# Kernel optimization log

Hardware: AMD Instinct MI355X
Metric: run time of the kernel (lower is better)

The kernel has to match this reference:

```python
import jax, jax.numpy as jnp
import numpy as np

BS, N, HID, INPUT, PREK, KHOP = 16, 1024, 64, 64, 4, 3
D = 2 * HID            # hidden channel dim (128)
F = 2 * INPUT          # input feature dim (128)
C = F + D              # graphconv input channels (256)
NM = KHOP + 1          # num_metrics = k_hop*n_supports + 1 with n_supports=1
PI = 3.141592653589793
EMB_RANGE = (12.0 + 2.0) / HID   # (gamma + epsilon) / hidden_size


def setup_inputs() -> dict:
    key = jax.random.key(0)
    ks = jax.random.split(key, 12)
    inputs = jax.random.normal(ks[0], (BS, N, F), jnp.float32)
    # per-sample dynamic support; scale by 1/N to keep Chebyshev recursion stable
    supports = jax.random.uniform(ks[1], (BS, N, N), jnp.float32) / N
    hidden_states = jax.random.normal(ks[2], (BS, PREK, N, D), jnp.float32)
    W = jax.random.normal(ks[3], (D, D), jnp.float32) * 0.02
    b = jax.random.normal(ks[4], (N, D), jnp.float32) * 0.02
    R = jax.random.normal(ks[5], (PREK, N, HID), jnp.float32) * 0.02
    gc_w = jax.random.normal(ks[6], (D, C * NM), jnp.float32) * 0.02
    gc_b = jax.random.normal(ks[7], (D,), jnp.float32) * 0.02
    ev_att_w = jax.random.normal(ks[8], (1, N * D), jnp.float32) * 0.001
    ev_att_b = jax.random.normal(ks[9], (1,), jnp.float32) * 0.02
    att_w = jax.random.normal(ks[10], (1, N * D), jnp.float32) * 0.001
    att_b = jax.random.normal(ks[11], (1,), jnp.float32) * 0.02
    return {"inputs": inputs, "supports": supports, "hidden_states": hidden_states,
            "W": W, "b": b, "R": R, "gc_w": gc_w, "gc_b": gc_b,
            "ev_att_w": ev_att_w, "ev_att_b": ev_att_b,
            "att_w": att_w, "att_b": att_b}


def reference(inputs, supports, hidden_states, W, b, R, gc_w, gc_b,
              ev_att_w, ev_att_b, att_w, att_b):
    bs, k, n, d = hidden_states.shape
    # split inputs / last hidden into real/imag halves
    re_in, im_in = jnp.split(inputs, 2, axis=-1)          # [bs,n,INPUT]
    preH = hidden_states[:, -1]                           # [bs,n,d]
    re_p, im_p = jnp.split(preH, 2, axis=-1)              # [bs,n,HID]
    conv_in = jnp.concatenate([re_in, re_p, im_in, im_p], axis=-1)  # [bs,n,C]

    # diffusion graph conv (Chebyshev-style recursion over single batched support)
    x0 = conv_in
    x1 = jnp.matmul(supports, x0)                         # [bs,n,C]
    xs = [x0, x1]
    for _ in range(2, KHOP + 1):
        x2 = 2.0 * jnp.matmul(supports, x1) - x0
        xs.append(x2)
        x0, x1 = x1, x2
    # stack K metrics, permute to [bs,n,C,K], flatten (channel-major, step-minor)
    x = jnp.stack(xs, axis=0).transpose(1, 2, 3, 0).reshape(bs, n, C * NM)
    gco = x @ gc_w.T + gc_b                               # [bs,n,d]

    # EvolutionCell attention over g=1 group (kept for faithfulness)
    xe = gco.reshape(bs, 1, n * d)
    se = xe @ ev_att_w.T + ev_att_b                       # [bs,1,1]
    we = jax.nn.softmax(se, axis=1)
    conv_out = (xe * we).sum(axis=1).reshape(bs, n, d)

    # leaky_relu_ (slope 0.01)
    conv_out = jnp.where(conv_out >= 0, conv_out, 0.01 * conv_out)

    # RotatE-style complex phase rotation of hidden states
    phase = R / (EMB_RANGE / PI)                          # [k,n,HID]
    re_rel, im_rel = jnp.cos(phase), jnp.sin(phase)
    re_h, im_h = jnp.split(hidden_states, 2, axis=-1)     # [bs,k,n,HID]
    re_new = re_rel * re_h - im_rel * im_h
    im_new = im_rel * re_h + re_rel * im_h
    new_states = jnp.concatenate([re_new, im_new], axis=-1)  # [bs,k,n,d]

    # attention over k memory slots
    xa = new_states.reshape(bs, k, n * d)
    sa = xa @ att_w.T + att_b                             # [bs,k,1]
    wa = jax.nn.softmax(sa, axis=1)
    att = (xa * wa).sum(axis=1).reshape(bs, n, d)

    output = conv_out @ W + b[None] + att                 # [bs,n,d]
    new_hidden = jnp.concatenate([hidden_states[:, 1:], output[:, None]], axis=1)
    return output, new_hidden
```

## Files before the change

### kernel.cpp

```cpp
#include <hip/hip_runtime.h>
#include <cstddef>

constexpr float PHASE_SCALE = (float)(3.141592653589793 / ((12.0 + 2.0) / 64.0));

typedef __bf16 bf16;
typedef __bf16 bf16x4 __attribute__((ext_vector_type(4)));
typedef __bf16 bf16x8 __attribute__((ext_vector_type(8)));
typedef float floatx4 __attribute__((ext_vector_type(4)));

#define GLOAD_LDS16(gp, lp) __builtin_amdgcn_global_load_lds( \
    (const __attribute__((address_space(1))) void*)(gp),      \
    (__attribute__((address_space(3))) void*)(lp), 16, 0, 0)

#define VM_WAIT(n) asm volatile("s_waitcnt vmcnt(" #n ")" ::: "memory")

__global__ __launch_bounds__(256) void prep_kernel(
    const float4* __restrict__ S, bf16* __restrict__ Sbf,
    const float* __restrict__ R,
    const float* __restrict__ gcw, const float* __restrict__ W,
    bf16* __restrict__ gtAll, bf16* __restrict__ WT,
    const float* __restrict__ inp, const float* __restrict__ hs,
    bf16* __restrict__ xRow, bf16* __restrict__ xT0,
    const float* __restrict__ attw, float* __restrict__ part)
{
    __shared__ bf16 tile[64][65];
    __shared__ float red[256];
    const int bid = blockIdx.x;
    const int tid = threadIdx.x;

    if (bid < 576) {
        int gi = bid * 256 + tid;
        if (gi < 131072) {
            int m = gi >> 15;
            int rem = gi & 32767;
            int d = rem >> 8;
            int c = rem & 255;
            gtAll[gi] = (bf16)gcw[(size_t)d * 1024 + c * 4 + m];
        } else {
            int r = gi - 131072;
            int n = r >> 7, k = r & 127;
            WT[r] = (bf16)W[(size_t)k * 128 + n];
        }
    } else if (bid < 1088) {
        int bid3 = bid - 576;
        int bk = bid3 & 63;
        int k = bk & 3;
        int chunk = bid3 >> 6;
        const float* hbase = hs + (size_t)bk * 131072;
        float acc = 0.f;
        for (int idx = tid; idx < 2048; idx += 256) {
            int h4 = (idx & 15) * 4;
            int n = chunk * 128 + (idx >> 4);
            float4 rr  = *(const float4*)(R + (size_t)k * 65536 + n * 64 + h4);
            float4 re  = *(const float4*)(hbase + (size_t)n * 128 + h4);
            float4 im  = *(const float4*)(hbase + (size_t)n * 128 + 64 + h4);
            float4 wre = *(const float4*)(attw + (size_t)n * 128 + h4);
            float4 wim = *(const float4*)(attw + (size_t)n * 128 + 64 + h4);
            float sv, cv;
            __sincosf(rr.x * PHASE_SCALE, &sv, &cv);
            acc += (cv * re.x - sv * im.x) * wre.x + (sv * re.x + cv * im.x) * wim.x;
            __sincosf(rr.y * PHASE_SCALE, &sv, &cv);
            acc += (cv * re.y - sv * im.y) * wre.y + (sv * re.y + cv * im.y) * wim.y;
            __sincosf(rr.z * PHASE_SCALE, &sv, &cv);
            acc += (cv * re.z - sv * im.z) * wre.z + (sv * re.z + cv * im.z) * wim.z;
            __sincosf(rr.w * PHASE_SCALE, &sv, &cv);
            acc += (cv * re.w - sv * im.w) * wre.w + (sv * re.w + cv * im.w) * wim.w;
        }
        red[tid] = acc;
        __syncthreads();
        for (int s2 = 128; s2 > 0; s2 >>= 1) {
            if (tid < s2) red[tid] += red[tid + s2];
            __syncthreads();
        }
        if (tid == 0) part[bk * 8 + chunk] = red[0];
    } else if (bid < 2112) {
        int lin = bid - 1088;
        int b = lin >> 6, by = (lin >> 2) & 15, bx = lin & 3;
        int n0 = by * 64, c0 = bx * 64;
        const float* base = (bx & 1) ? (hs + (((size_t)b * 4 + 3) * 1024) * 128)
                                     : (inp + ((size_t)b * 1024) * 128);
        int soff = (bx >> 1) * 64;
        #pragma unroll
        for (int it = 0; it < 2; ++it) {
            int unit = it * 256 + tid;
            int nl = unit >> 3, cs = unit & 7;
            const float* src = base + (size_t)(n0 + nl) * 128 + soff + cs * 8;
            float4 a0 = *(const float4*)src;
            float4 a1 = *(const float4*)(src + 4);
            bf16x8 o;
            o[0] = (bf16)a0.x; o[1] = (bf16)a0.y; o[2] = (bf16)a0.z; o[3] = (bf16)a0.w;
            o[4] = (bf16)a1.x; o[5] = (bf16)a1.y; o[6] = (bf16)a1.z; o[7] = (bf16)a1.w;
            *(bf16x8*)(xRow + ((size_t)b * 1024 + n0 + nl) * 256 + c0 + cs * 8) = o;
            #pragma unroll
            for (int e = 0; e < 8; ++e) tile[nl][cs * 8 + e] = o[e];
        }
        __syncthreads();
        #pragma unroll
        for (int it = 0; it < 4; ++it) {
            int unit = it * 256 + tid;
            int ng = unit & 15, cc = unit >> 4;
            bf16x4 v;
            #pragma unroll
            for (int r = 0; r < 4; ++r) v[r] = tile[ng * 4 + r][cc];
            *(bf16x4*)(xT0 + ((size_t)b * 256 + c0 + cc) * 1024 + n0 + ng * 4) = v;
        }
    } else {
        int gi = (bid - 2112) * 256 + tid;
        const float4* Sp = S + (size_t)gi * 2;
        float4 v0 = Sp[0];
        float4 v1 = Sp[1];
        bf16x8 o;
        o[0] = (bf16)v0.x; o[1] = (bf16)v0.y; o[2] = (bf16)v0.z; o[3] = (bf16)v0.w;
        o[4] = (bf16)v1.x; o[5] = (bf16)v1.y; o[6] = (bf16)v1.z; o[7] = (bf16)v1.w;
        *(bf16x8*)(Sbf + (size_t)gi * 8) = o;
    }
}

__global__ __launch_bounds__(512) void cheb_mfma_kernel(
    const bf16* __restrict__ S, const bf16* __restrict__ xT,
    const bf16* __restrict__ xTprev, bf16* __restrict__ outT,
    const bf16* __restrict__ xRow0, const bf16* __restrict__ gtA,
    const bf16* __restrict__ gt0, float* __restrict__ gcoF,
    float alpha, int accumulate)
{
    __shared__ char smem[122880];
    const int f = blockIdx.x;
    const int b = (f & 7) + 8 * ((f >> 3) & 1);
    const int n0 = (f >> 4) * 64;
    const int tid = threadIdx.x;
    const int wave = tid >> 6, lane = tid & 63;
    const int wr = (wave & 3) * 16;
    const int wc = (wave >> 2) * 128;
    const int l15 = lane & 15, quad = lane >> 4;
    const int lrow = lane >> 3;
    const int segsw = (lane & 7) ^ lrow;

    const bf16* Sb = S + (size_t)b * 1048576;
    const bf16* xb = xT + (size_t)b * 262144;

    auto stage = [&](int buf, int k0) {
        bf16* dA = (bf16*)(smem + buf * 40960);
        bf16* dB = dA + 4096;
        {
            const bf16* gp = Sb + (size_t)(n0 + wave * 8 + lrow) * 1024 + k0 + segsw * 8;
            GLOAD_LDS16(gp, dA + wave * 8 * 64);
        }
        #pragma unroll
        for (int v = 0; v < 4; ++v) {
            int cq = wave * 32 + v * 8;
            const bf16* gp = xb + (size_t)(cq + lrow) * 1024 + k0 + segsw * 8;
            GLOAD_LDS16(gp, dB + cq * 64);
        }
    };

    floatx4 acc[8] = {};
    stage(0, 0);
    stage(1, 64);
    for (int i = 0; i < 16; ++i) {
        if (i < 15) { VM_WAIT(5); } else { VM_WAIT(0); }
        __builtin_amdgcn_s_barrier();
        __builtin_amdgcn_sched_barrier(0);
        const bf16* lA = (const bf16*)(smem + (i % 3) * 40960);
        const bf16* lB = lA + 4096;
        #pragma unroll
        for (int ks = 0; ks < 2; ++ks) {
            int row = wr + l15;
            int aslot = (ks * 4 + quad) ^ (row & 7);
            bf16x8 af = *(const bf16x8*)(lA + row * 64 + aslot * 8);
            #pragma unroll
            for (int j = 0; j < 8; ++j) {
                int col = wc + j * 16 + l15;
                int bslot = (ks * 4 + quad) ^ (col & 7);
                bf16x8 bfr = *(const bf16x8*)(lB + col * 64 + bslot * 8);
                acc[j] = __builtin_amdgcn_mfma_f32_16x16x32_bf16(af, bfr, acc[j], 0, 0, 0);
            }
        }
        if (i + 2 < 16) stage((i + 2) % 3, (i + 2) * 64);
    }

    const bf16* pT = xTprev ? xTprev + (size_t)b * 262144 : nullptr;
    bf16* oT = outT ? outT + (size_t)b * 262144 : nullptr;
    bf16x4 xo[8];
    #pragma unroll
    for (int j = 0; j < 8; ++j) {
        int col = wc + j * 16 + l15;
        float v[4];
        #pragma unroll
        for (int r = 0; r < 4; ++r) v[r] = alpha * acc[j][r];
        if (pT) {
            bf16x4 pp = *(const bf16x4*)(pT + (size_t)col * 1024 + n0 + wr + quad * 4);
            #pragma unroll
            for (int r = 0; r < 4; ++r) v[r] -= (float)pp[r];
        }
        #pragma unroll
        for (int r = 0; r < 4; ++r) xo[j][r] = (bf16)v[r];
        if (oT) *(bf16x4*)(oT + (size_t)col * 1024 + n0 + wr + quad * 4) = xo[j];
    }

    __syncthreads();
    bf16* ldsX = (bf16*)smem;
    #pragma unroll
    for (int j = 0; j < 8; ++j) {
        int col = wc + j * 16 + l15;
        #pragma unroll
        for (int r = 0; r < 4; ++r)
            ldsX[(wr + quad * 4 + r) * 264 + col] = xo[j][r];
    }
    __syncthreads();

    const int dbase = (wave >> 2) * 64;
    floatx4 a2[4] = {};
    for (int k2 = 0; k2 < 256; k2 += 32) {
        bf16x8 af = *(const bf16x8*)(ldsX + (wr + l15) * 264 + k2 + quad * 8);
        #pragma unroll
        for (int j = 0; j < 4; ++j) {
            int dcol = dbase + j * 16 + l15;
            bf16x8 bfr = *(const bf16x8*)(gtA + (size_t)dcol * 256 + k2 + quad * 8);
            a2[j] = __builtin_amdgcn_mfma_f32_16x16x32_bf16(af, bfr, a2[j], 0, 0, 0);
        }
    }
    if (xRow0) {
        for (int k2 = 0; k2 < 256; k2 += 32) {
            bf16x8 af = *(const bf16x8*)(xRow0 + ((size_t)b * 1024 + n0 + wr + l15) * 256 + k2 + quad * 8);
            #pragma unroll
            for (int j = 0; j < 4; ++j) {
                int dcol = dbase + j * 16 + l15;
                bf16x8 bfr = *(const bf16x8*)(gt0 + (size_t)dcol * 256 + k2 + quad * 8);
                a2[j] = __builtin_amdgcn_mfma_f32_16x16x32_bf16(af, bfr, a2[j], 0, 0, 0);
            }
        }
    }
    #pragma unroll
    for (int j = 0; j < 4; ++j) {
        int dcol = dbase + j * 16 + l15;
        #pragma unroll
        for (int r = 0; r < 4; ++r) {
            size_t idx = ((size_t)b * 1024 + n0 + wr + quad * 4 + r) * 128 + dcol;
            if (accumulate) gcoF[idx] += a2[j][r];
            else            gcoF[idx]  = a2[j][r];
        }
    }
}

__global__ __launch_bounds__(256) void final_kernel(
    const float* __restrict__ gcoF, const float* __restrict__ gcb,
    const bf16* __restrict__ WT, const float* __restrict__ bvec,
    const float* __restrict__ hs, const float* __restrict__ R,
    const float* __restrict__ part, const float* __restrict__ attb,
    float* __restrict__ out, float* __restrict__ newh)
{
    const int m0 = blockIdx.x * 64;
    const int b = m0 >> 10, n0 = m0 & 1023;
    const int tid = threadIdx.x;
    const int wave = tid >> 6, lane = tid & 63;
    const int l15 = lane & 15, quad = lane >> 4;

    const int arow = m0 + wave * 16 + l15;
    floatx4 acc[8] = {};
    #pragma unroll
    for (int k0 = 0; k0 < 128; k0 += 32) {
        int kk = k0 + quad * 8;
        float4 p0 = *(const float4*)(gcoF + (size_t)arow * 128 + kk);
        float4 p1 = *(const float4*)(gcoF + (size_t)arow * 128 + kk + 4);
        float4 g0 = *(const float4*)(gcb + kk);
        float4 g1 = *(const float4*)(gcb + kk + 4);
        float vv[8] = {p0.x + g0.x, p0.y + g0.y, p0.z + g0.z, p0.w + g0.w,
                       p1.x + g1.x, p1.y + g1.y, p1.z + g1.z, p1.w + g1.w};
        bf16x8 af;
        #pragma unroll
        for (int e = 0; e < 8; ++e) {
            float v = vv[e];
            af[e] = (bf16)(v >= 0.f ? v : 0.01f * v);
        }
        #pragma unroll
        for (int j = 0; j < 8; ++j) {
            bf16x8 bfr = *(const bf16x8*)(WT + (size_t)(j * 16 + l15) * 128 + kk);
            acc[j] = __builtin_amdgcn_mfma_f32_16x16x32_bf16(af, bfr, acc[j], 0, 0, 0);
        }
    }

    float sa[4], mx = -1e30f;
    #pragma unroll
    for (int k = 0; k < 4; ++k) {
        float s = attb[0];
        #pragma unroll
        for (int c = 0; c < 8; ++c) s += part[(b * 4 + k) * 8 + c];
        sa[k] = s;
        mx = fmaxf(mx, s);
    }
    float den = 0.f;
    #pragma unroll
    for (int k = 0; k < 4; ++k) { sa[k] = __expf(sa[k] - mx); den += sa[k]; }
    float inv = 1.f / den;
    #pragma unroll
    for (int k = 0; k < 4; ++k) sa[k] *= inv;

    #pragma unroll
    for (int jj = 0; jj < 4; ++jj) {
        int hcol = jj * 16 + l15;
        #pragma unroll
        for (int r = 0; r < 4; ++r) {
            int n = n0 + wave * 16 + quad * 4 + r;
            float attRe = 0.f, attIm = 0.f;
            #pragma unroll
            for (int k = 0; k < 4; ++k) {
                const float* hb = hs + (((size_t)(b * 4 + k) * 1024 + n) * 128);
                float re = hb[hcol], im = hb[64 + hcol];
                float s, c;
                __sincosf(R[(size_t)k * 65536 + n * 64 + hcol] * PHASE_SCALE, &s, &c);
                attRe += sa[k] * (c * re - s * im);
                attIm += sa[k] * (s * re + c * im);
                if (k >= 1) {
                    size_t nb = (size_t)b * 524288 + (size_t)(k - 1) * 131072 + (size_t)n * 128;
                    newh[nb + hcol] = re;
                    newh[nb + 64 + hcol] = im;
                }
            }
            size_t ob = (size_t)(m0 + wave * 16 + quad * 4 + r) * 128;
            float oRe = acc[jj][r]     + bvec[(size_t)n * 128 + hcol]      + attRe;
            float oIm = acc[jj + 4][r] + bvec[(size_t)n * 128 + 64 + hcol] + attIm;
            out[ob + hcol] = oRe;
            out[ob + 64 + hcol] = oIm;
            size_t nb3 = (size_t)b * 524288 + 393216 + (size_t)n * 128;
            newh[nb3 + hcol] = oRe;
            newh[nb3 + 64 + hcol] = oIm;
        }
    }
}

extern "C" void kernel_launch(void* const* d_in, const int* in_sizes, int n_in,
                              void* d_out, int out_size, void* d_ws, size_t ws_size,
                              hipStream_t stream) {
    const float* inp  = (const float*)d_in[0];
    const float* sup  = (const float*)d_in[1];
    const float* hs   = (const float*)d_in[2];
    const float* W    = (const float*)d_in[3];
    const float* bvec = (const float*)d_in[4];
    const float* R    = (const float*)d_in[5];
    const float* gcw  = (const float*)d_in[6];
    const float* gcb  = (const float*)d_in[7];
    const float* attw = (const float*)d_in[10];
    const float* attb = (const float*)d_in[11];

    float* out  = (float*)d_out;
    float* newh = out + 2097152;
    bf16*  Sbf  = (bf16*)newh;

    char* w = (char*)d_ws;
    bf16*  xT0   = (bf16*)(w);
    bf16*  xT1   = (bf16*)(w + 8388608);
    bf16*  xT2   = (bf16*)(w + 16777216);
    bf16*  xRow  = (bf16*)(w + 25165824);
    float* gcoF  = (float*)(w + 33554432);
    bf16*  gtAll = (bf16*)(w + 41943040);
    bf16*  WT    = (bf16*)(w + 42205184);
    float* part  = (float*)(w + 42237952);

    prep_kernel<<<10304, 256, 0, stream>>>((const float4*)sup, Sbf, R, gcw, W,
                                           gtAll, WT, inp, hs, xRow, xT0, attw, part);

    cheb_mfma_kernel<<<256, 512, 0, stream>>>(Sbf, xT0, nullptr, xT1,
                                              xRow, gtAll + 32768, gtAll, gcoF, 1.0f, 0);
    cheb_mfma_kernel<<<256, 512, 0, stream>>>(Sbf, xT1, xT0, xT2,
                                              nullptr, gtAll + 2 * 32768, nullptr, gcoF, 2.0f, 1);
    cheb_mfma_kernel<<<256, 512, 0, stream>>>(Sbf, xT2, xT1, nullptr,
                                              nullptr, gtAll + 3 * 32768, nullptr, gcoF, 2.0f, 1);

    final_kernel<<<256, 256, 0, stream>>>(gcoF, gcb, WT, bvec, hs, R, part, attb, out, newh);
}
```

Baseline: 262.8 us.

## Deepen cheb GEMM prefetch to four LDS buffers and split final kernel finer

The Chebyshev MFMA kernel now keeps three tiles in flight across four LDS buffers (160KB) instead of two across three, which should hide more global-load latency. The final kernel is remapped so each block handles 16 rows instead of 64, with every wave computing one 16-column slice, which gives 1024 blocks instead of 256. The aim is more memory-level parallelism and better occupancy across the CUs. The risk is that the larger LDS footprint still limits residency to one block per CU, and the smaller final blocks reload WT and the softmax partials more often.

```diff
diff --git a/kernel.cpp b/kernel.cpp
--- a/kernel.cpp
+++ b/kernel.cpp
@@ -123,7 +123,7 @@
     const bf16* __restrict__ gt0, float* __restrict__ gcoF,
     float alpha, int accumulate)
 {
-    __shared__ char smem[122880];
+    __shared__ char smem[163840];
     const int f = blockIdx.x;
     const int b = (f & 7) + 8 * ((f >> 3) & 1);
     const int n0 = (f >> 4) * 64;
@@ -156,11 +156,14 @@
     floatx4 acc[8] = {};
     stage(0, 0);
     stage(1, 64);
+    stage(2, 128);
     for (int i = 0; i < 16; ++i) {
-        if (i < 15) { VM_WAIT(5); } else { VM_WAIT(0); }
+        if (i < 14)      { VM_WAIT(10); }
+        else if (i == 14){ VM_WAIT(5); }
+        else             { VM_WAIT(0); }
         __builtin_amdgcn_s_barrier();
         __builtin_amdgcn_sched_barrier(0);
-        const bf16* lA = (const bf16*)(smem + (i % 3) * 40960);
+        const bf16* lA = (const bf16*)(smem + (i & 3) * 40960);
         const bf16* lB = lA + 4096;
         #pragma unroll
         for (int ks = 0; ks < 2; ++ks) {
@@ -175,7 +178,7 @@
                 acc[j] = __builtin_amdgcn_mfma_f32_16x16x32_bf16(af, bfr, acc[j], 0, 0, 0);
             }
         }
-        if (i + 2 < 16) stage((i + 2) % 3, (i + 2) * 64);
+        if (i + 3 < 16) stage((i + 3) & 3, (i + 3) * 64);
     }
 
     const bf16* pT = xTprev ? xTprev + (size_t)b * 262144 : nullptr;
@@ -249,19 +252,18 @@
     const float* __restrict__ part, const float* __restrict__ attb,
     float* __restrict__ out, float* __restrict__ newh)
 {
-    const int m0 = blockIdx.x * 64;
+    const int m0 = blockIdx.x * 16;
     const int b = m0 >> 10, n0 = m0 & 1023;
     const int tid = threadIdx.x;
     const int wave = tid >> 6, lane = tid & 63;
     const int l15 = lane & 15, quad = lane >> 4;
 
-    const int arow = m0 + wave * 16 + l15;
-    floatx4 acc[8] = {};
+    floatx4 acc0 = {}, acc1 = {};
     #pragma unroll
     for (int k0 = 0; k0 < 128; k0 += 32) {
         int kk = k0 + quad * 8;
-        float4 p0 = *(const float4*)(gcoF + (size_t)arow * 128 + kk);
-        float4 p1 = *(const float4*)(gcoF + (size_t)arow * 128 + kk + 4);
+        float4 p0 = *(const float4*)(gcoF + (size_t)(m0 + l15) * 128 + kk);
+        float4 p1 = *(const float4*)(gcoF + (size_t)(m0 + l15) * 128 + kk + 4);
         float4 g0 = *(const float4*)(gcb + kk);
         float4 g1 = *(const float4*)(gcb + kk + 4);
         float vv[8] = {p0.x + g0.x, p0.y + g0.y, p0.z + g0.z, p0.w + g0.w,
@@ -272,11 +274,10 @@
             float v = vv[e];
             af[e] = (bf16)(v >= 0.f ? v : 0.01f * v);
         }
-        #pragma unroll
-        for (int j = 0; j < 8; ++j) {
-            bf16x8 bfr = *(const bf16x8*)(WT + (size_t)(j * 16 + l15) * 128 + kk);
-            acc[j] = __builtin_amdgcn_mfma_f32_16x16x32_bf16(af, bfr, acc[j], 0, 0, 0);
-        }
+        bf16x8 b0 = *(const bf16x8*)(WT + (size_t)(wave * 16 + l15) * 128 + kk);
+        bf16x8 b1 = *(const bf16x8*)(WT + (size_t)(64 + wave * 16 + l15) * 128 + kk);
+        acc0 = __builtin_amdgcn_mfma_f32_16x16x32_bf16(af, b0, acc0, 0, 0, 0);
+        acc1 = __builtin_amdgcn_mfma_f32_16x16x32_bf16(af, b1, acc1, 0, 0, 0);
     }
 
     float sa[4], mx = -1e30f;
@@ -295,36 +296,33 @@
     #pragma unroll
     for (int k = 0; k < 4; ++k) sa[k] *= inv;
 
-    #pragma unroll
-    for (int jj = 0; jj < 4; ++jj) {
-        int hcol = jj * 16 + l15;
-        #pragma unroll
-        for (int r = 0; r < 4; ++r) {
-            int n = n0 + wave * 16 + quad * 4 + r;
-            float attRe = 0.f, attIm = 0.f;
-            #pragma unroll
-            for (int k = 0; k < 4; ++k) {
-                const float* hb = hs + (((size_t)(b * 4 + k) * 1024 + n) * 128);
-                float re = hb[hcol], im = hb[64 + hcol];
-                float s, c;
-                __sincosf(R[(size_t)k * 65536 + n * 64 + hcol] * PHASE_SCALE, &s, &c);
-                attRe += sa[k] * (c * re - s * im);
-                attIm += sa[k] * (s * re + c * im);
-                if (k >= 1) {
-                    size_t nb = (size_t)b * 524288 + (size_t)(k - 1) * 131072 + (size_t)n * 128;
-                    newh[nb + hcol] = re;
-                    newh[nb + 64 + hcol] = im;
-                }
+    const int hcol = wave * 16 + l15;
+    #pragma unroll
+    for (int r = 0; r < 4; ++r) {
+        int n = n0 + quad * 4 + r;
+        float attRe = 0.f, attIm = 0.f;
+        #pragma unroll
+        for (int k = 0; k < 4; ++k) {
+            const float* hb = hs + (((size_t)(b * 4 + k) * 1024 + n) * 128);
+            float re = hb[hcol], im = hb[64 + hcol];
+            float s, c;
+            __sincosf(R[(size_t)k * 65536 + n * 64 + hcol] * PHASE_SCALE, &s, &c);
+            attRe += sa[k] * (c * re - s * im);
+            attIm += sa[k] * (s * re + c * im);
+            if (k >= 1) {
+                size_t nb = (size_t)b * 524288 + (size_t)(k - 1) * 131072 + (size_t)n * 128;
+                newh[nb + hcol] = re;
+                newh[nb + 64 + hcol] = im;
             }
-            size_t ob = (size_t)(m0 + wave * 16 + quad * 4 + r) * 128;
-            float oRe = acc[jj][r]     + bvec[(size_t)n * 128 + hcol]      + attRe;
-            float oIm = acc[jj + 4][r] + bvec[(size_t)n * 128 + 64 + hcol] + attIm;
-            out[ob + hcol] = oRe;
-            out[ob + 64 + hcol] = oIm;
-            size_t nb3 = (size_t)b * 524288 + 393216 + (size_t)n * 128;
-            newh[nb3 + hcol] = oRe;
-            newh[nb3 + 64 + hcol] = oIm;
-        }
+        }
+        size_t ob = (size_t)(m0 + quad * 4 + r) * 128;
+        float oRe = acc0[r] + bvec[(size_t)n * 128 + hcol]      + attRe;
+        float oIm = acc1[r] + bvec[(size_t)n * 128 + 64 + hcol] + attIm;
+        out[ob + hcol] = oRe;
+        out[ob + 64 + hcol] = oIm;
+        size_t nb3 = (size_t)b * 524288 + 393216 + (size_t)n * 128;
+        newh[nb3 + hcol] = oRe;
+        newh[nb3 + 64 + hcol] = oIm;
     }
 }
 
@@ -366,5 +364,5 @@
     cheb_mfma_kernel<<<256, 512, 0, stream>>>(Sbf, xT2, xT1, nullptr,
                                               nullptr, gtAll + 3 * 32768, nullptr, gcoF, 2.0f, 1);
 
-    final_kernel<<<256, 256, 0, stream>>>(gcoF, gcb, WT, bvec, hs, R, part, attb, out, newh);
+    final_kernel<<<1024, 256, 0, stream>>>(gcoF, gcb, WT, bvec, hs, R, part, attb, out, newh);
 }
```

After: 267.4 us. No clear change (+1.7%).
